# Performance work log

Measured on AMD Instinct MI355X. Metric: run time of the kernel, lower is better.

Reference implementation:

```python
import jax, jax.numpy as jnp
import numpy as np

B, CIN, COUT, H, W = 8, 128, 128, 64, 64

# kernel-grid base offsets (dy, dx), row-major k = kh*3 + kw, matching torch base_offset-1
BASE = jnp.array([[-1, -1], [-1, 0], [-1, 1],
                  [0, -1], [0, 0], [0, 1],
                  [1, -1], [1, 0], [1, 1]], dtype=jnp.float32)  # [9,2]
CORNER = jnp.array([1, 0, 1, 0, 0, 0, 1, 0, 1], dtype=jnp.float32)  # mask1 per kernel tap
EDGE = jnp.array([0, 1, 0, 1, 0, 1, 0, 1, 0], dtype=jnp.float32)    # mask2 per kernel tap


def conv3x3(x, w, b=None):
    out = jax.lax.conv_general_dilated(
        x, w, window_strides=(1, 1), padding=((1, 1), (1, 1)),
        dimension_numbers=('NCHW', 'OIHW', 'NCHW'))
    if b is not None:
        out = out + b[None, :, None, None]
    return out


def bilinear_sample(x, py, px):
    Bv, C, Hin, Win = x.shape
    y0 = jnp.floor(py)
    x0 = jnp.floor(px)
    wy = py - y0
    wx = px - x0
    y0i = y0.astype(jnp.int32)
    x0i = x0.astype(jnp.int32)
    xf = x.reshape(Bv, C, Hin * Win)

    def corner(yi, xi):
        valid = ((yi >= 0) & (yi < Hin) & (xi >= 0) & (xi < Win)).astype(x.dtype)
        idx = jnp.clip(yi, 0, Hin - 1) * Win + jnp.clip(xi, 0, Win - 1)  # [B,K,Ho,Wo]
        g = jax.vmap(lambda xb, ib: xb[:, ib])(xf, idx)  # [B,C,K,Ho,Wo]
        return g * valid[:, None]

    v00 = corner(y0i, x0i)
    v01 = corner(y0i, x0i + 1)
    v10 = corner(y0i + 1, x0i)
    v11 = corner(y0i + 1, x0i + 1)
    wy = wy[:, None]
    wx = wx[:, None]
    return (v00 * (1 - wy) * (1 - wx) + v01 * (1 - wy) * wx
            + v10 * wy * (1 - wx) + v11 * wy * wx)


def setup_inputs() -> dict:
    key = jax.random.key(0)
    k1, k2, k3 = jax.random.split(key, 3)
    x = jax.random.normal(k1, (B, CIN, H, W), dtype=jnp.float32)
    # small offset-conv weights keep predicted offsets in a realistic sub-pixel range
    w_off = jax.random.normal(k2, (5, CIN, 3, 3), dtype=jnp.float32) * 0.02
    b_off = jnp.zeros((5,), dtype=jnp.float32)
    w = jax.random.normal(k3, (COUT, CIN, 3, 3), dtype=jnp.float32) * (1.0 / np.sqrt(CIN * 9))
    b = jnp.zeros((COUT,), dtype=jnp.float32)
    return {"x": x, "w_off": w_off, "b_off": b_off, "w": w, "b": b}


def reference(x, w_off, b_off, w, b):
    off = conv3x3(x, w_off, b_off)          # [B,5,H,W]
    scale1 = jax.nn.relu(off[:, 2:3]) + 1.0  # corner scale [B,1,H,W]
    scale2 = jax.nn.relu(off[:, 3:4]) + 1.0  # edge scale   [B,1,H,W]
    shift = off[:, :2]                       # equivariant shift vector [B,2,H,W]

    # per-tap scale; center tap gets 0 but its base offset is (0,0) anyway
    scale_k = CORNER[None, :, None, None] * scale1 + EDGE[None, :, None, None] * scale2  # [B,9,H,W]
    # deform offset = scaled_base - base + shift = base*(scale-1) + shift
    delta = BASE[None, :, :, None, None] * (scale_k - 1.0)[:, :, None] + shift[:, None]  # [B,9,2,H,W]

    hs = jnp.arange(H, dtype=x.dtype)
    ws = jnp.arange(W, dtype=x.dtype)
    # sampling positions: p0 + base_k + offset_k (stride=1, pad=1)
    py = hs[None, None, :, None] + BASE[None, :, 0, None, None] + delta[:, :, 0]  # [B,9,H,W]
    px = ws[None, None, None, :] + BASE[None, :, 1, None, None] + delta[:, :, 1]

    sampled = bilinear_sample(x, py, px)  # [B,CIN,9,H,W]
    out = jnp.einsum('bckhw,ock->bohw', sampled, w.reshape(COUT, CIN, 9))
    return out + b[None, :, None, None]
```

## Files before the change

kernel.cpp:

```cpp
#include <hip/hip_runtime.h>

#define Wd 64
#define Hd 64
#define HWp 4096
#define CIN_ 128
#define COUT_ 128

typedef __bf16 bf16x8 __attribute__((ext_vector_type(8)));
typedef float f32x4 __attribute__((ext_vector_type(4)));

__device__ inline ushort f2bf(float f) {
    unsigned u = __float_as_uint(f);
    u += 0x7fff + ((u >> 16) & 1);
    return (ushort)(u >> 16);
}
__device__ inline float bflo(unsigned u) { return __uint_as_float(u << 16); }
__device__ inline float bfhi(unsigned u) { return __uint_as_float(u & 0xffff0000u); }
__device__ inline unsigned bfround(float f) {
    unsigned u = __float_as_uint(f);
    return u + 0x7fff + ((u >> 16) & 1);
}
__device__ inline unsigned pack2(float lo, float hi) {
    return __builtin_amdgcn_perm(bfround(hi), bfround(lo), 0x07060302);
}

__global__ __launch_bounds__(256) void prep_offsets_kernel(
    const float* __restrict__ x, const float* __restrict__ w,
    const float* __restrict__ w_off, const float* __restrict__ b_off,
    ushort* __restrict__ xt, ushort* __restrict__ w_t2,
    int4* __restrict__ midx, float4* __restrict__ mw)
{
    __shared__ char smem[34816];
    int blk = blockIdx.x;
    int t = threadIdx.x;

    if (blk < 256) {
        ushort* tile = (ushort*)smem;
        int b = blk >> 5, yx0 = (blk & 31) << 7;
        const float* xb = x + (size_t)b * CIN_ * HWp + yx0;
        int lanelo = t & 31, grp = t >> 5;
        #pragma unroll
        for (int i = 0; i < 4; i++) {
            int cbase = i * 32 + grp * 4;
            float4 v0 = *(const float4*)(xb + (size_t)(cbase + 0) * HWp + lanelo * 4);
            float4 v1 = *(const float4*)(xb + (size_t)(cbase + 1) * HWp + lanelo * 4);
            float4 v2 = *(const float4*)(xb + (size_t)(cbase + 2) * HWp + lanelo * 4);
            float4 v3 = *(const float4*)(xb + (size_t)(cbase + 3) * HWp + lanelo * 4);
            ushort4 u;
            u.x = f2bf(v0.x); u.y = f2bf(v1.x); u.z = f2bf(v2.x); u.w = f2bf(v3.x);
            *(ushort4*)&tile[(lanelo * 4 + 0) * 136 + cbase] = u;
            u.x = f2bf(v0.y); u.y = f2bf(v1.y); u.z = f2bf(v2.y); u.w = f2bf(v3.y);
            *(ushort4*)&tile[(lanelo * 4 + 1) * 136 + cbase] = u;
            u.x = f2bf(v0.z); u.y = f2bf(v1.z); u.z = f2bf(v2.z); u.w = f2bf(v3.z);
            *(ushort4*)&tile[(lanelo * 4 + 2) * 136 + cbase] = u;
            u.x = f2bf(v0.w); u.y = f2bf(v1.w); u.z = f2bf(v2.w); u.w = f2bf(v3.w);
            *(ushort4*)&tile[(lanelo * 4 + 3) * 136 + cbase] = u;
        }
        __syncthreads();
        ushort* dst = xt + ((size_t)b * HWp + yx0) * CIN_;
        int c8 = (t & 15) * 8, yxg = t >> 4;
        #pragma unroll
        for (int i = 0; i < 8; i++) {
            int yxl = i * 16 + yxg;
            int4 v = *(int4*)&tile[yxl * 136 + c8];
            *(int4*)(dst + (size_t)yxl * CIN_ + c8) = v;
        }
    } else if (blk < 832) {
        int i = (blk - 256) * 256 + t;
        int j    = i & 7;
        int lane = (i >> 3) & 63;
        int ii   = (i >> 9) & 3;
        int wm   = (i >> 11) & 1;
        int s    = i >> 12;
        int o = wm * 64 + ii * 16 + (lane & 15);
        int c = (s & 3) * 32 + (lane >> 4) * 8 + j;
        int k = s >> 2;
        w_t2[i] = f2bf(w[o * 1152 + c * 9 + k]);
    } else {
        float* wl   = (float*)smem;
        float* part = (float*)(smem + 18432);
        float* der  = (float*)(smem + 22528);
        int blk2 = blk - 832;
        int b = blk2 >> 6;
        int h = blk2 & 63;

        for (int i = t; i < 4608; i += 256) {
            int j = i / 1152;
            int r = i - j * 1152;
            wl[r * 4 + j] = w_off[i];
        }
        __syncthreads();

        int pi = t & 63, cc = t >> 6;
        const float* xb = x + (size_t)(b * CIN_ + cc * 32) * HWp;

        int idx9[9];
        float msk9[9];
        #pragma unroll
        for (int dy = 0; dy < 3; dy++) {
            int hy = h + dy - 1;
            int hyc = min(max(hy, 0), Hd - 1);
            bool vr = (hy >= 0) && (hy < Hd);
            #pragma unroll
            for (int dx = 0; dx < 3; dx++) {
                int wx = pi + dx - 1;
                int wxc = min(max(wx, 0), Wd - 1);
                bool v = vr && (wx >= 0) && (wx < Wd);
                idx9[dy * 3 + dx] = hyc * Wd + wxc;
                msk9[dy * 3 + dx] = v ? 1.0f : 0.0f;
            }
        }

        float o0 = 0.f, o1 = 0.f, o2 = 0.f, o3 = 0.f;
        #pragma unroll 2
        for (int c = 0; c < 32; c++) {
            const float* xp = xb + c * HWp;
            const float* wc = &wl[(cc * 32 + c) * 36];
            float xv[9];
            #pragma unroll
            for (int tp = 0; tp < 9; tp++) xv[tp] = xp[idx9[tp]] * msk9[tp];
            #pragma unroll
            for (int tp = 0; tp < 9; tp++) {
                float4 wj = *(const float4*)&wc[tp * 4];
                o0 += xv[tp] * wj.x; o1 += xv[tp] * wj.y;
                o2 += xv[tp] * wj.z; o3 += xv[tp] * wj.w;
            }
        }
        part[t * 4 + 0] = o0;
        part[t * 4 + 1] = o1;
        part[t * 4 + 2] = o2;
        part[t * 4 + 3] = o3;
        __syncthreads();

        if (t < 64) {
            float s0 = b_off[0], s1 = b_off[1], s2 = b_off[2], s3 = b_off[3];
            #pragma unroll
            for (int q = 0; q < 4; q++) {
                s0 += part[(q * 64 + t) * 4 + 0];
                s1 += part[(q * 64 + t) * 4 + 1];
                s2 += part[(q * 64 + t) * 4 + 2];
                s3 += part[(q * 64 + t) * 4 + 3];
            }
            der[t * 4 + 0] = s0;
            der[t * 4 + 1] = s1;
            der[t * 4 + 2] = fmaxf(s2, 0.f) + 1.f;
            der[t * 4 + 3] = fmaxf(s3, 0.f) + 1.f;
        }
        __syncthreads();

        #pragma unroll
        for (int s = 0; s < 3; s++) {
            int q = t + s * 256;
            if (q < 576) {
                int k = q >> 6;
                int pp = q & 63;
                float sy = der[pp * 4 + 0], sx = der[pp * 4 + 1];
                float sc1 = der[pp * 4 + 2], sc2 = der[pp * 4 + 3];
                int ky = k / 3, kx = k - ky * 3;
                float by = (float)(ky - 1), bx = (float)(kx - 1);
                bool corner = (ky != 1) && (kx != 1);
                bool edge = (ky != 1) ^ (kx != 1);
                float sk = corner ? sc1 : (edge ? sc2 : 0.0f);
                float py = (float)h + by * sk + sy;
                float px = (float)pp + bx * sk + sx;
                float y0f = floorf(py), x0f = floorf(px);
                float wy = py - y0f, wx = px - x0f;
                int y0 = (int)y0f, x0 = (int)x0f;
                int y1 = y0 + 1, x1 = x0 + 1;
                float vy0 = (y0 >= 0 && y0 < Hd) ? 1.f : 0.f;
                float vy1 = (y1 >= 0 && y1 < Hd) ? 1.f : 0.f;
                float vx0 = (x0 >= 0 && x0 < Wd) ? 1.f : 0.f;
                float vx1 = (x1 >= 0 && x1 < Wd) ? 1.f : 0.f;
                int cy0 = min(max(y0, 0), Hd - 1), cy1 = min(max(y1, 0), Hd - 1);
                int cx0 = min(max(x0, 0), Wd - 1), cx1 = min(max(x1, 0), Wd - 1);
                int4 ii;
                ii.x = cy0 * Wd + cx0;
                ii.y = cy0 * Wd + cx1;
                ii.z = cy1 * Wd + cx0;
                ii.w = cy1 * Wd + cx1;
                float4 ww;
                ww.x = (1.f - wy) * (1.f - wx) * vy0 * vx0;
                ww.y = (1.f - wy) * wx * vy0 * vx1;
                ww.z = wy * (1.f - wx) * vy1 * vx0;
                ww.w = wy * wx * vy1 * vx1;
                int addr = (b * 9 + k) * HWp + h * Wd + pp;
                midx[addr] = ii;
                mw[addr] = ww;
            }
        }
    }
}

struct Gath { int4 g0, g1, g2, g3; int4 a0, a1, a2, a3; };

__global__ __launch_bounds__(256, 2) void deform_gemm_mfma(
    const ushort* __restrict__ xt, const ushort* __restrict__ w_t2,
    const float* __restrict__ bias, const int4* __restrict__ midx,
    const float4* __restrict__ mw, float* __restrict__ out)
{
    __shared__ ushort S_lds[2][64 * 40];

    int t = threadIdx.x;
    int b = blockIdx.x >> 6;
    int h = blockIdx.x & 63;
    int p0 = h << 6;
    const ushort* xtb = xt + (size_t)b * HWp * CIN_;

    int p = t >> 2;
    int c8 = (t & 3) << 3;

    int wv = t >> 6, lane = t & 63;
    int wm = wv & 1, wn = wv >> 1;
    int lm = lane & 15, lq = lane >> 4;

    f32x4 acc[4][2] = {};

    int4 mi = midx[(b * 9 + 0) * HWp + p0 + p];
    float4 mv = mw[(b * 9 + 0) * HWp + p0 + p];

    auto issue = [&](int s) -> Gath {
        int q = s & 3;
        const ushort* base = xtb + q * 32 + c8;
        Gath r;
        r.g0 = *(const int4*)(base + mi.x * CIN_);
        r.g1 = *(const int4*)(base + mi.y * CIN_);
        r.g2 = *(const int4*)(base + mi.z * CIN_);
        r.g3 = *(const int4*)(base + mi.w * CIN_);
        const ushort* ab = w_t2 + (size_t)(((s * 2 + wm) * 4) * 64 + lane) * 8;
        r.a0 = *(const int4*)(ab);
        r.a1 = *(const int4*)(ab + 512);
        r.a2 = *(const int4*)(ab + 1024);
        r.a3 = *(const int4*)(ab + 1536);
        return r;
    };
    auto commitS = [&](int nb, const Gath& G) {
        const unsigned* u0 = (const unsigned*)&G.g0;
        const unsigned* u1 = (const unsigned*)&G.g1;
        const unsigned* u2 = (const unsigned*)&G.g2;
        const unsigned* u3 = (const unsigned*)&G.g3;
        unsigned sd[4];
        #pragma unroll
        for (int d = 0; d < 4; d++) {
            float vlo = mv.x * bflo(u0[d]) + mv.y * bflo(u1[d])
                      + mv.z * bflo(u2[d]) + mv.w * bflo(u3[d]);
            float vhi = mv.x * bfhi(u0[d]) + mv.y * bfhi(u1[d])
                      + mv.z * bfhi(u2[d]) + mv.w * bfhi(u3[d]);
            sd[d] = pack2(vlo, vhi);
        }
        *(int4*)&S_lds[nb][p * 40 + c8] = *(const int4*)sd;
    };

    Gath Gc = issue(0);
    commitS(0, Gc);
    __syncthreads();

    for (int s = 0; s < 36; s++) {
        int cur = s & 1;
        bool prod = (s + 1 < 36);
        Gath Gn;
        if (prod) {
            if (((s + 1) & 3) == 0) {
                int k = (s + 1) >> 2;
                mi = midx[(b * 9 + k) * HWp + p0 + p];
                mv = mw[(b * 9 + k) * HWp + p0 + p];
            }
            Gn = issue(s + 1);
        }

        bf16x8 bfr[2];
        #pragma unroll
        for (int j = 0; j < 2; j++)
            bfr[j] = *(const bf16x8*)&S_lds[cur][(wn * 32 + j * 16 + lm) * 40 + lq * 8];
        bf16x8 af[4];
        af[0] = *(const bf16x8*)&Gc.a0;
        af[1] = *(const bf16x8*)&Gc.a1;
        af[2] = *(const bf16x8*)&Gc.a2;
        af[3] = *(const bf16x8*)&Gc.a3;
        #pragma unroll
        for (int i = 0; i < 4; i++)
            #pragma unroll
            for (int j = 0; j < 2; j++)
                acc[i][j] = __builtin_amdgcn_mfma_f32_16x16x32_bf16(
                    af[i], bfr[j], acc[i][j], 0, 0, 0);

        if (prod) {
            commitS(cur ^ 1, Gn);
            Gc = Gn;
        }
        __syncthreads();
    }

    #pragma unroll
    for (int i = 0; i < 4; i++) {
        #pragma unroll
        for (int r = 0; r < 4; r++) {
            int o = wm * 64 + i * 16 + lq * 4 + r;
            float bv = bias[o];
            float* orow = out + (size_t)(b * COUT_ + o) * HWp + p0 + wn * 32 + lm;
            #pragma unroll
            for (int j = 0; j < 2; j++)
                orow[j * 16] = acc[i][j][r] + bv;
        }
    }
}

extern "C" void kernel_launch(void* const* d_in, const int* in_sizes, int n_in,
                              void* d_out, int out_size, void* d_ws, size_t ws_size,
                              hipStream_t stream) {
    const float* x     = (const float*)d_in[0];
    const float* w_off = (const float*)d_in[1];
    const float* b_off = (const float*)d_in[2];
    const float* w     = (const float*)d_in[3];
    const float* bias  = (const float*)d_in[4];
    float* out = (float*)d_out;

    char* ws = (char*)d_ws;
    ushort* xt   = (ushort*)ws;
    ushort* w_t2 = (ushort*)(ws + 8388608);
    int4*   midx = (int4*)(ws + 8683520);
    float4* mwp  = (float4*)(ws + 13402112);

    prep_offsets_kernel<<<1344, 256, 0, stream>>>(x, w, w_off, b_off,
                                                  xt, w_t2, midx, mwp);
    deform_gemm_mfma<<<512, 256, 0, stream>>>(xt, w_t2, bias, midx, mwp, out);
}
```

Baseline: 130.2 us.

## Gather bilinear samples directly into MFMA B fragments in fp16, drop LDS staging

```diff
diff --git a/kernel.cpp b/kernel.cpp
--- a/kernel.cpp
+++ b/kernel.cpp
@@ -6,23 +6,24 @@
 #define CIN_ 128
 #define COUT_ 128
 
-typedef __bf16 bf16x8 __attribute__((ext_vector_type(8)));
-typedef float f32x4 __attribute__((ext_vector_type(4)));
-
-__device__ inline ushort f2bf(float f) {
-    unsigned u = __float_as_uint(f);
-    u += 0x7fff + ((u >> 16) & 1);
-    return (ushort)(u >> 16);
-}
-__device__ inline float bflo(unsigned u) { return __uint_as_float(u << 16); }
-__device__ inline float bfhi(unsigned u) { return __uint_as_float(u & 0xffff0000u); }
-__device__ inline unsigned bfround(float f) {
-    unsigned u = __float_as_uint(f);
-    return u + 0x7fff + ((u >> 16) & 1);
-}
-__device__ inline unsigned pack2(float lo, float hi) {
-    return __builtin_amdgcn_perm(bfround(hi), bfround(lo), 0x07060302);
-}
+typedef _Float16 f16;
+typedef _Float16 h2   __attribute__((ext_vector_type(2)));
+typedef _Float16 f16x8 __attribute__((ext_vector_type(8)));
+typedef float f32x4   __attribute__((ext_vector_type(4)));
+
+__device__ inline ushort f2h(float f) {
+    f16 h = (f16)f;
+    return __builtin_bit_cast(ushort, h);
+}
+__device__ inline h2 gb(const int4& g, int d) {
+    return __builtin_bit_cast(h2, (&g.x)[d]);
+}
+__device__ inline h2 dup(float f) {
+    f16 h = (f16)f;
+    h2 r; r[0] = h; r[1] = h;
+    return r;
+}
+struct H8 { h2 r[4]; };
 
 __global__ __launch_bounds__(256) void prep_offsets_kernel(
     const float* __restrict__ x, const float* __restrict__ w,
@@ -47,13 +48,13 @@
             float4 v2 = *(const float4*)(xb + (size_t)(cbase + 2) * HWp + lanelo * 4);
             float4 v3 = *(const float4*)(xb + (size_t)(cbase + 3) * HWp + lanelo * 4);
             ushort4 u;
-            u.x = f2bf(v0.x); u.y = f2bf(v1.x); u.z = f2bf(v2.x); u.w = f2bf(v3.x);
+            u.x = f2h(v0.x); u.y = f2h(v1.x); u.z = f2h(v2.x); u.w = f2h(v3.x);
             *(ushort4*)&tile[(lanelo * 4 + 0) * 136 + cbase] = u;
-            u.x = f2bf(v0.y); u.y = f2bf(v1.y); u.z = f2bf(v2.y); u.w = f2bf(v3.y);
+            u.x = f2h(v0.y); u.y = f2h(v1.y); u.z = f2h(v2.y); u.w = f2h(v3.y);
             *(ushort4*)&tile[(lanelo * 4 + 1) * 136 + cbase] = u;
-            u.x = f2bf(v0.z); u.y = f2bf(v1.z); u.z = f2bf(v2.z); u.w = f2bf(v3.z);
+            u.x = f2h(v0.z); u.y = f2h(v1.z); u.z = f2h(v2.z); u.w = f2h(v3.z);
             *(ushort4*)&tile[(lanelo * 4 + 2) * 136 + cbase] = u;
-            u.x = f2bf(v0.w); u.y = f2bf(v1.w); u.z = f2bf(v2.w); u.w = f2bf(v3.w);
+            u.x = f2h(v0.w); u.y = f2h(v1.w); u.z = f2h(v2.w); u.w = f2h(v3.w);
             *(ushort4*)&tile[(lanelo * 4 + 3) * 136 + cbase] = u;
         }
         __syncthreads();
@@ -75,7 +76,7 @@
         int o = wm * 64 + ii * 16 + (lane & 15);
         int c = (s & 3) * 32 + (lane >> 4) * 8 + j;
         int k = s >> 2;
-        w_t2[i] = f2bf(w[o * 1152 + c * 9 + k]);
+        w_t2[i] = f2h(w[o * 1152 + c * 9 + k]);
     } else {
         float* wl   = (float*)smem;
         float* part = (float*)(smem + 18432);
@@ -191,103 +192,102 @@
     }
 }
 
-struct Gath { int4 g0, g1, g2, g3; int4 a0, a1, a2, a3; };
-
 __global__ __launch_bounds__(256, 2) void deform_gemm_mfma(
     const ushort* __restrict__ xt, const ushort* __restrict__ w_t2,
     const float* __restrict__ bias, const int4* __restrict__ midx,
     const float4* __restrict__ mw, float* __restrict__ out)
 {
-    __shared__ ushort S_lds[2][64 * 40];
-
     int t = threadIdx.x;
     int b = blockIdx.x >> 6;
     int h = blockIdx.x & 63;
     int p0 = h << 6;
     const ushort* xtb = xt + (size_t)b * HWp * CIN_;
 
-    int p = t >> 2;
-    int c8 = (t & 3) << 3;
-
     int wv = t >> 6, lane = t & 63;
-    int wm = wv & 1, wn = wv >> 1;
+    int wm = wv & 1, ns = wv >> 1;
     int lm = lane & 15, lq = lane >> 4;
 
     f32x4 acc[4][2] = {};
 
-    int4 mi = midx[(b * 9 + 0) * HWp + p0 + p];
-    float4 mv = mw[(b * 9 + 0) * HWp + p0 + p];
-
-    auto issue = [&](int s) -> Gath {
+    const ushort* cb[2][4];
+    h2 cw[2][4];
+    auto loadmeta = [&](int k) {
+        #pragma unroll
+        for (int f = 0; f < 2; f++) {
+            int addr = (b * 9 + k) * HWp + p0 + ns * 32 + f * 16 + lm;
+            int4 mi = midx[addr];
+            float4 v = mw[addr];
+            cb[f][0] = xtb + mi.x * CIN_ + lq * 8;
+            cb[f][1] = xtb + mi.y * CIN_ + lq * 8;
+            cb[f][2] = xtb + mi.z * CIN_ + lq * 8;
+            cb[f][3] = xtb + mi.w * CIN_ + lq * 8;
+            cw[f][0] = dup(v.x); cw[f][1] = dup(v.y);
+            cw[f][2] = dup(v.z); cw[f][3] = dup(v.w);
+        }
+    };
+
+    int4 Gc[2][4], Gn[2][4];
+    f16x8 Ac[4], An[4];
+    h2 Wc[2][4], Wn[2][4];
+
+    auto issue = [&](int s, int4 G[2][4], f16x8 A[4], h2 W[2][4]) {
         int q = s & 3;
-        const ushort* base = xtb + q * 32 + c8;
-        Gath r;
-        r.g0 = *(const int4*)(base + mi.x * CIN_);
-        r.g1 = *(const int4*)(base + mi.y * CIN_);
-        r.g2 = *(const int4*)(base + mi.z * CIN_);
-        r.g3 = *(const int4*)(base + mi.w * CIN_);
-        const ushort* ab = w_t2 + (size_t)(((s * 2 + wm) * 4) * 64 + lane) * 8;
-        r.a0 = *(const int4*)(ab);
-        r.a1 = *(const int4*)(ab + 512);
-        r.a2 = *(const int4*)(ab + 1024);
-        r.a3 = *(const int4*)(ab + 1536);
-        return r;
+        #pragma unroll
+        for (int f = 0; f < 2; f++)
+            #pragma unroll
+            for (int r = 0; r < 4; r++) {
+                G[f][r] = *(const int4*)(cb[f][r] + q * 32);
+                W[f][r] = cw[f][r];
+            }
+        const ushort* ab = w_t2 + (size_t)((s * 2 + wm) * 4 * 64 + lane) * 8;
+        #pragma unroll
+        for (int i = 0; i < 4; i++)
+            A[i] = *(const f16x8*)(ab + i * 512);
     };
-    auto commitS = [&](int nb, const Gath& G) {
-        const unsigned* u0 = (const unsigned*)&G.g0;
-        const unsigned* u1 = (const unsigned*)&G.g1;
-        const unsigned* u2 = (const unsigned*)&G.g2;
-        const unsigned* u3 = (const unsigned*)&G.g3;
-        unsigned sd[4];
-        #pragma unroll
-        for (int d = 0; d < 4; d++) {
-            float vlo = mv.x * bflo(u0[d]) + mv.y * bflo(u1[d])
-                      + mv.z * bflo(u2[d]) + mv.w * bflo(u3[d]);
-            float vhi = mv.x * bfhi(u0[d]) + mv.y * bfhi(u1[d])
-                      + mv.z * bfhi(u2[d]) + mv.w * bfhi(u3[d]);
-            sd[d] = pack2(vlo, vhi);
-        }
-        *(int4*)&S_lds[nb][p * 40 + c8] = *(const int4*)sd;
-    };
-
-    Gath Gc = issue(0);
-    commitS(0, Gc);
-    __syncthreads();
+
+    loadmeta(0);
+    issue(0, Gc, Ac, Wc);
 
     for (int s = 0; s < 36; s++) {
-        int cur = s & 1;
         bool prod = (s + 1 < 36);
-        Gath Gn;
         if (prod) {
-            if (((s + 1) & 3) == 0) {
-                int k = (s + 1) >> 2;
-                mi = midx[(b * 9 + k) * HWp + p0 + p];
-                mv = mw[(b * 9 + k) * HWp + p0 + p];
-            }
-            Gn = issue(s + 1);
-        }
-
-        bf16x8 bfr[2];
-        #pragma unroll
-        for (int j = 0; j < 2; j++)
-            bfr[j] = *(const bf16x8*)&S_lds[cur][(wn * 32 + j * 16 + lm) * 40 + lq * 8];
-        bf16x8 af[4];
-        af[0] = *(const bf16x8*)&Gc.a0;
-        af[1] = *(const bf16x8*)&Gc.a1;
-        af[2] = *(const bf16x8*)&Gc.a2;
-        af[3] = *(const bf16x8*)&Gc.a3;
+            if (((s + 1) & 3) == 0) loadmeta((s + 1) >> 2);
+            issue(s + 1, Gn, An, Wn);
+        }
+
+        f16x8 bfr[2];
+        #pragma unroll
+        for (int f = 0; f < 2; f++) {
+            H8 tmp;
+            #pragma unroll
+            for (int d = 0; d < 4; d++) {
+                h2 r = gb(Gc[f][0], d) * Wc[f][0];
+                r = gb(Gc[f][1], d) * Wc[f][1] + r;
+                r = gb(Gc[f][2], d) * Wc[f][2] + r;
+                r = gb(Gc[f][3], d) * Wc[f][3] + r;
+                tmp.r[d] = r;
+            }
+            bfr[f] = __builtin_bit_cast(f16x8, tmp);
+        }
+
         #pragma unroll
         for (int i = 0; i < 4; i++)
             #pragma unroll
-            for (int j = 0; j < 2; j++)
-                acc[i][j] = __builtin_amdgcn_mfma_f32_16x16x32_bf16(
-                    af[i], bfr[j], acc[i][j], 0, 0, 0);
+            for (int f = 0; f < 2; f++)
+                acc[i][f] = __builtin_amdgcn_mfma_f32_16x16x32_f16(
+                    Ac[i], bfr[f], acc[i][f], 0, 0, 0);
 
         if (prod) {
-            commitS(cur ^ 1, Gn);
-            Gc = Gn;
-        }
-        __syncthreads();
+            #pragma unroll
+            for (int f = 0; f < 2; f++)
+                #pragma unroll
+                for (int r = 0; r < 4; r++) {
+                    Gc[f][r] = Gn[f][r];
+                    Wc[f][r] = Wn[f][r];
+                }
+            #pragma unroll
+            for (int i = 0; i < 4; i++) Ac[i] = An[i];
+        }
     }
 
     #pragma unroll
@@ -296,10 +296,10 @@
         for (int r = 0; r < 4; r++) {
             int o = wm * 64 + i * 16 + lq * 4 + r;
             float bv = bias[o];
-            float* orow = out + (size_t)(b * COUT_ + o) * HWp + p0 + wn * 32 + lm;
-            #pragma unroll
-            for (int j = 0; j < 2; j++)
-                orow[j * 16] = acc[i][j][r] + bv;
+            float* orow = out + (size_t)(b * COUT_ + o) * HWp + p0 + ns * 32 + lm;
+            #pragma unroll
+            for (int f = 0; f < 2; f++)
+                orow[f * 16] = acc[i][f][r] + bv;
         }
     }
 }
```

After: 163.6 us. 1.26x slower.
